# Performance work log

Measured on AMD Instinct MI355X. Metric: run time of the kernel, lower is better.

## Reference

```python
import jax, jax.numpy as jnp
import numpy as np

N_LAT, N_LON = 121, 240
N = N_LAT * N_LON          # 29040 nodes (fixed by module's reshape)
DEG = 16
E = N * DEG                # 464640 edges
H = 128                    # input_nf = output_nf = hidden_nf
LV = 11                    # pressure levels (coord_mlp outputs 11*2)
EDGE_IN = 2 * H + 34       # source + target + w_diff(33) + edge_attr(1)


def setup_inputs() -> dict:
    key = jax.random.key(0)
    ks = jax.random.split(key, 18)
    def w(k, shape, s=0.05):
        return jax.random.normal(k, shape, dtype=jnp.float32) * s
    return {
        'h': w(ks[0], (N, H), 1.0),
        'u': w(ks[1], (N, LV), 1.0),
        'v': w(ks[2], (N, LV), 1.0),
        'edge_attr': w(ks[3], (E, 1), 1.0),
        # edge MLP: Linear(EDGE_IN,H) ReLU Linear(H,H) ReLU
        'W_e1': w(ks[4], (EDGE_IN, H)), 'b_e1': jnp.zeros((H,), jnp.float32),
        'W_e2': w(ks[5], (H, H)),       'b_e2': jnp.zeros((H,), jnp.float32),
        # node MLP: Linear(2H+H,H) ReLU Linear(H,H)
        'W_n1': w(ks[6], (3 * H, H)),   'b_n1': jnp.zeros((H,), jnp.float32),
        'W_n2': w(ks[7], (H, H)),       'b_n2': jnp.zeros((H,), jnp.float32),
        # coord MLP: Linear(H,H) ReLU Linear(H,22,bias=False) with tiny xavier gain
        'W_c1': w(ks[8], (H, H)),       'b_c1': jnp.zeros((H,), jnp.float32),
        'W_cl': w(ks[9], (H, 2 * LV), 0.001),
        'edge_index': jax.random.randint(ks[10], (2, E), 0, N, dtype=jnp.int32),
    }


def reference(h, u, v, edge_attr,
              W_e1, b_e1, W_e2, b_e2,
              W_n1, b_n1, W_n2, b_n2,
              W_c1, b_c1, W_cl,
              edge_index):
    row, col = edge_index[0], edge_index[1]

    # ---- coord2radial ----
    uc, vc = u[col], v[col]          # [E, LV]
    ur, vr = u[row], v[row]
    col_speed = jnp.sqrt(uc * uc + vc * vc)
    row_speed = jnp.sqrt(ur * ur + vr * vr)
    rel_dirt = (uc * ur + vc * vr) / (col_speed * row_speed)
    w_diff = jnp.concatenate([rel_dirt, col_speed, row_speed], axis=1)  # [E, 33]

    # ---- edge model ----
    edge_in = jnp.concatenate([h[row], h[col], w_diff, edge_attr], axis=1)  # [E, EDGE_IN]
    edge_feat = jax.nn.relu(jax.nn.relu(edge_in @ W_e1 + b_e1) @ W_e2 + b_e2)  # [E, H]

    # ---- node model (scatter-sum + lat-band mean pooling) ----
    agg = jax.ops.segment_sum(edge_feat, row, num_segments=N)  # [N, H]
    lat = agg.reshape(N_LAT, N_LON, H).mean(axis=1, keepdims=True)  # [121,1,H]
    lat_agg = jnp.broadcast_to(lat, (N_LAT, N_LON, H)).reshape(N, H)
    node_in = jnp.concatenate([h, agg, lat_agg], axis=1)  # [N, 3H]
    h_out = jax.nn.relu(node_in @ W_n1 + b_n1) @ W_n2 + b_n2 + h  # residual

    # ---- coord model (scatter-mean with clamp) ----
    ef = (jax.nn.relu(edge_feat @ W_c1 + b_c1) @ W_cl).reshape(E, 2, LV)
    radial = jnp.stack([uc, vc], axis=1)                 # [E, 2, LV]
    rad2 = jnp.sqrt(jnp.sum(radial * radial, axis=-1))   # [E, 2] (per-component magnitude)
    wind = ef * rad2[:, :, None]                         # [E, 2, LV]
    cnt = jnp.maximum(
        jax.ops.segment_sum(jnp.ones((E,), jnp.float32), row, num_segments=N), 1.0)[:, None]
    agg_u = jnp.clip(jax.ops.segment_sum(wind[:, 0, :], row, num_segments=N) / cnt, -100.0, 100.0)
    agg_v = jnp.clip(jax.ops.segment_sum(wind[:, 1, :], row, num_segments=N) / cnt, -100.0, 100.0)

    return h_out, agg_u, agg_v
```

## Files before the change

### kernel.cpp

```cpp
#include <hip/hip_runtime.h>
#include <hip/hip_bf16.h>
#include <math.h>

#define NN   29040
#define NLAT 121
#define NLON 240
#define HD   128
#define LVN  11
#define EE   464640

typedef __attribute__((ext_vector_type(8))) short short8;
typedef __attribute__((ext_vector_type(16))) float f16v;

#define OFF_WE1 0
#define OFF_WE2 40960
#define OFF_WC1 57344
#define OFF_WCL 73728
#define OFF_WN1 77824
#define OFF_WN2 126976
#define WP_SHORTS 143360

__device__ inline short f2b(float x) {
    union { __hip_bfloat16 b; short s; } v;
    v.b = __float2bfloat16(x);
    return v.s;
}
__device__ inline float b2f(unsigned short b) {
    union { unsigned u; float f; } v; v.u = ((unsigned)b) << 16;
    return v.f;
}

#define SB_HIST  1815
#define SB_HCAST 1815
#define SB_UV    114
#define SB_WP    70

__global__ __launch_bounds__(256)
void setup_kernel(const int* __restrict__ eidx, int* __restrict__ cnt,
                  const float* __restrict__ h, short* __restrict__ hb,
                  const float* __restrict__ u, const float* __restrict__ v,
                  short* __restrict__ uvb,
                  const float* __restrict__ We1, const float* __restrict__ We2,
                  const float* __restrict__ Wc1, const float* __restrict__ Wcl,
                  const float* __restrict__ Wn1, const float* __restrict__ Wn2,
                  short* __restrict__ wp)
{
    const int b = blockIdx.x, tid = threadIdx.x;
    if (b < SB_HIST) {
        int e = b * 256 + tid;
        atomicAdd(&cnt[eidx[e]], 1);
        return;
    }
    if (b < SB_HIST + SB_HCAST) {
        int idx = (b - SB_HIST) * 256 + tid;
        const float4* hf = (const float4*)h;
        float4 a = hf[idx * 2], c = hf[idx * 2 + 1];
        short8 o;
        o[0] = f2b(a.x); o[1] = f2b(a.y); o[2] = f2b(a.z); o[3] = f2b(a.w);
        o[4] = f2b(c.x); o[5] = f2b(c.y); o[6] = f2b(c.z); o[7] = f2b(c.w);
        ((short8*)hb)[idx] = o;
        return;
    }
    if (b < SB_HIST + SB_HCAST + SB_UV) {
        int n = (b - SB_HIST - SB_HCAST) * 256 + tid;
        if (n >= NN) return;
        short* r = uvb + (size_t)n * 40;
        float un = 0.f, vn = 0.f;
#pragma unroll
        for (int l = 0; l < LVN; ++l) {
            float uu = u[n * LVN + l], vv = v[n * LVN + l];
            float s = sqrtf(uu * uu + vv * vv);
            r[l]      = f2b(uu / s);
            r[11 + l] = f2b(vv / s);
            r[22 + l] = f2b(s);
            un += uu * uu; vn += vv * vv;
        }
        r[33] = f2b(sqrtf(un));
        r[34] = f2b(sqrtf(vn));
        r[35] = 0; r[36] = 0; r[37] = 0; r[38] = 0; r[39] = 0;
        return;
    }
    {
        int fg = (b - SB_HIST - SB_HCAST - SB_UV) * 4 + (tid >> 6);
        const int l = tid & 63;
        int kind, f, base;
        if (fg < 80)       { kind = 0; f = fg;       base = OFF_WE1; }
        else if (fg < 112) { kind = 1; f = fg - 80;  base = OFF_WE2; }
        else if (fg < 144) { kind = 2; f = fg - 112; base = OFF_WC1; }
        else if (fg < 152) { kind = 3; f = fg - 144; base = OFF_WCL; }
        else if (fg < 248) { kind = 4; f = fg - 152; base = OFF_WN1; }
        else               { kind = 5; f = fg - 248; base = OFF_WN2; }
        const int nfw = (kind == 3) ? 1 : 4;
        const int kf = f / nfw, nf = f % nfw;
        short* dst = wp + base + (size_t)f * 512 + l * 8;
        for (int i = 0; i < 8; ++i) {
            int k = kf * 16 + ((l >> 5) << 3) + i;
            int n = nf * 32 + (l & 31);
            float val = 0.f;
            if (kind == 0) {
                int r = (k < 33) ? (256 + k) : (k == 33 ? 289 : (k < 64 ? -1 : k - 64));
                if (r >= 0) val = We1[r * HD + n];
            } else if (kind == 1) val = We2[k * HD + n];
            else if (kind == 2)  val = Wc1[k * HD + n];
            else if (kind == 3)  { if (n < 22) val = Wcl[k * 22 + n]; }
            else if (kind == 4)  val = Wn1[k * HD + n];
            else                 val = Wn2[k * HD + n];
            dst[i] = f2b(val);
        }
    }
}

__global__ __launch_bounds__(1024)
void scan_kernel(const int* __restrict__ cnt, int* __restrict__ off)
{
    __shared__ int part[1024];
    const int tid = threadIdx.x;
    const int CH = 29;
    int lo = tid * CH, hi = min(lo + CH, NN);
    int s = 0;
    for (int i = lo; i < hi; ++i) s += cnt[i];
    part[tid] = s;
    __syncthreads();
    for (int d = 1; d < 1024; d <<= 1) {
        int vv = (tid >= d) ? part[tid - d] : 0;
        __syncthreads();
        part[tid] += vv;
        __syncthreads();
    }
    int run = (tid == 0) ? 0 : part[tid - 1];
    for (int i = lo; i < hi; ++i) { off[i] = run; run += cnt[i]; }
    if (tid == 1023) off[NN] = run;
}

__global__ __launch_bounds__(256)
void scatter_kernel(const int* __restrict__ eidx, const float* __restrict__ ea,
                    const int* __restrict__ off, int* __restrict__ cur,
                    int* __restrict__ rows_r, int* __restrict__ cols_r,
                    float* __restrict__ ear)
{
    int e = blockIdx.x * 256 + threadIdx.x;
    if (e >= EE) return;
    int row = eidx[e];
    int col = eidx[EE + e];
    float a = ea[e];
    int p = atomicAdd(&cur[row], 1);
    int idx = off[row] + p;
    rows_r[idx] = row;
    cols_r[idx] = col;
    ear[idx] = a;
}

template<int KF, int NFL, int NJ>
__device__ inline void gemm32_lds(const short* At, const short* Wp, int nf0,
                                  const float* bias, f16v* acc,
                                  int mrow, int colbase, int r31, int kh, int lane)
{
    const char* arow = (const char*)At + mrow * 256;
    const int sw = (mrow & 7) << 4;
#pragma unroll
    for (int j = 0; j < NJ; ++j) {
        float bv = bias ? bias[colbase + j * 32 + r31] : 0.f;
#pragma unroll
        for (int q = 0; q < 16; ++q) acc[j][q] = bv;
    }
#pragma unroll
    for (int kf = 0; kf < KF; ++kf) {
        short8 a = *(const short8*)(arow + ((kf * 32 + 16 * kh) ^ sw));
#pragma unroll
        for (int j = 0; j < NJ; ++j) {
            short8 bfr = *(const short8*)(Wp + (size_t)(kf * NFL + nf0 + j) * 512 + lane * 8);
            acc[j] = __builtin_amdgcn_mfma_f32_32x32x16_bf16(a, bfr, acc[j], 0, 0, 0);
        }
    }
}

template<int NJ>
__device__ inline void store32(short* tile, const f16v* acc, int rg, int colbase,
                               int r31, int kh, bool relu)
{
#pragma unroll
    for (int j = 0; j < NJ; ++j)
#pragma unroll
        for (int reg = 0; reg < 16; ++reg) {
            int row = rg * 32 + (reg & 3) + 8 * (reg >> 2) + 4 * kh;
            int cb2 = (colbase + j * 32 + r31) * 2;
            float vv = acc[j][reg];
            if (relu) vv = fmaxf(vv, 0.f);
            *(short*)((char*)tile + row * 256 + (cb2 ^ ((row & 7) << 4))) = f2b(vv);
        }
}

__global__ __launch_bounds__(256, 4)
void edge_mfma(const short* __restrict__ hb, const short* __restrict__ uvb,
               const int* __restrict__ rows_r, const int* __restrict__ cols_r,
               const float* __restrict__ ear,
               const float* __restrict__ be1, const float* __restrict__ be2,
               const float* __restrict__ bc1,
               const short* __restrict__ wp,
               float* __restrict__ agg, float* __restrict__ aggu,
               float* __restrict__ aggv)
{
    __shared__ short Twd[64 * 64];
    __shared__ short T1[64 * 128];
    __shared__ int   rows_s[64];
    __shared__ float radu_s[64], radv_s[64];

    const int tid = threadIdx.x, lane = tid & 63, w = tid >> 6;
    const int rg = w >> 1, cg = w & 1;
    const int e0 = blockIdx.x * 64;
    const int r31 = lane & 31, kh = lane >> 5;
    const int mrow = rg * 32 + r31;
    const int sw = (mrow & 7) << 4;
    const int colbase = cg * 64;

    int rowm = rows_r[e0 + mrow], colm = cols_r[e0 + mrow];
    const short* hr = hb + (size_t)rowm * HD + 8 * kh;
    const short* hc = hb + (size_t)colm * HD + 8 * kh;

    {
        const int m2 = tid >> 2, q = tid & 3;
        const int sw2 = (m2 & 7) << 4;
        int row2 = rows_r[e0 + m2], col2 = cols_r[e0 + m2];
        const short* rc = uvb + (size_t)col2 * 40;
        const short* rr = uvb + (size_t)row2 * 40;
        char* arow = (char*)(Twd + m2 * 64);
        short8 z = {0, 0, 0, 0, 0, 0, 0, 0};
        *(short8*)(arow + q * 32) = z;
        *(short8*)(arow + q * 32 + 16) = z;
        for (int l = q; l < LVN; l += 4) {
            float rel = b2f((unsigned short)rc[l]) * b2f((unsigned short)rr[l])
                      + b2f((unsigned short)rc[11 + l]) * b2f((unsigned short)rr[11 + l]);
            *(short*)(arow + ((2 * l) ^ sw2))        = f2b(rel);
            *(short*)(arow + ((2 * (11 + l)) ^ sw2)) = rc[22 + l];
            *(short*)(arow + ((2 * (22 + l)) ^ sw2)) = rr[22 + l];
        }
        if (q == 0) {
            rows_s[m2] = row2;
            radu_s[m2] = b2f((unsigned short)rc[33]);
            radv_s[m2] = b2f((unsigned short)rc[34]);
        }
        if (q == 3) *(short*)(arow + ((2 * 33) ^ sw2)) = f2b(ear[e0 + m2]);
    }
    __syncthreads();

    f16v acc[2];
#pragma unroll
    for (int j = 0; j < 2; ++j) {
        float bv = be1[colbase + j * 32 + r31];
#pragma unroll
        for (int q = 0; q < 16; ++q) acc[j][q] = bv;
    }
    {
        const char* awd = (const char*)(Twd + mrow * 64);
#pragma unroll
        for (int kf = 0; kf < 4; ++kf) {
            short8 a = *(const short8*)(awd + ((kf * 32 + 16 * kh) ^ sw));
#pragma unroll
            for (int j = 0; j < 2; ++j) {
                short8 bfr = *(const short8*)(wp + OFF_WE1 + (size_t)(kf * 4 + cg * 2 + j) * 512 + lane * 8);
                acc[j] = __builtin_amdgcn_mfma_f32_32x32x16_bf16(a, bfr, acc[j], 0, 0, 0);
            }
        }
#pragma unroll
        for (int s = 0; s < 8; ++s) {
            short8 a = *(const short8*)(hr + s * 16);
#pragma unroll
            for (int j = 0; j < 2; ++j) {
                short8 bfr = *(const short8*)(wp + OFF_WE1 + (size_t)((s + 4) * 4 + cg * 2 + j) * 512 + lane * 8);
                acc[j] = __builtin_amdgcn_mfma_f32_32x32x16_bf16(a, bfr, acc[j], 0, 0, 0);
            }
        }
#pragma unroll
        for (int s = 0; s < 8; ++s) {
            short8 a = *(const short8*)(hc + s * 16);
#pragma unroll
            for (int j = 0; j < 2; ++j) {
                short8 bfr = *(const short8*)(wp + OFF_WE1 + (size_t)((s + 12) * 4 + cg * 2 + j) * 512 + lane * 8);
                acc[j] = __builtin_amdgcn_mfma_f32_32x32x16_bf16(a, bfr, acc[j], 0, 0, 0);
            }
        }
    }
    store32<2>(T1, acc, rg, colbase, r31, kh, true);
    __syncthreads();

    gemm32_lds<8, 4, 2>(T1, wp + OFF_WE2, cg * 2, be2, acc, mrow, colbase, r31, kh, lane);
    __syncthreads();
    store32<2>(T1, acc, rg, colbase, r31, kh, true);
    __syncthreads();

    gemm32_lds<8, 4, 2>(T1, wp + OFF_WC1, cg * 2, bc1, acc, mrow, colbase, r31, kh, lane);

    {
        const int col = colbase + lane;
        const int m0 = rg * 32;
        int curr = rows_s[m0];
        float s = 0.f;
        for (int m = m0; m < m0 + 32; ++m) {
            int r = rows_s[m];
            float vv = b2f(*(const unsigned short*)((const char*)T1 + m * 256 + (((col & 127) * 2) ^ ((m & 7) << 4))));
            if (r != curr) { atomicAdd(&agg[(size_t)curr * HD + (col & 127)], s); s = 0.f; curr = r; }
            s += vv;
        }
        atomicAdd(&agg[(size_t)curr * HD + (col & 127)], s);
    }
    __syncthreads();
    store32<2>(T1, acc, rg, colbase, r31, kh, true);
    __syncthreads();

    if (cg == 0) {
        gemm32_lds<8, 1, 1>(T1, wp + OFF_WCL, 0, (const float*)nullptr, acc, mrow, 0, r31, kh, lane);
        float* O22 = (float*)Twd;
#pragma unroll
        for (int reg = 0; reg < 16; ++reg) {
            int row = rg * 32 + (reg & 3) + 8 * (reg >> 2) + 4 * kh;
            O22[row * 32 + r31] = acc[0][reg];
        }
        const int c = r31;
        if (c < 22) {
            const bool isU = c < LVN;
            const int lvl = isU ? c : c - LVN;
            float* dst = isU ? aggu : aggv;
            const float* radp = isU ? radu_s : radv_s;
            const int m0 = rg * 32 + kh * 16;
            int curr = rows_s[m0]; float s = 0.f;
            for (int m = m0; m < m0 + 16; ++m) {
                int r = rows_s[m];
                float vv = O22[m * 32 + c] * radp[m];
                if (r != curr) { atomicAdd(&dst[(size_t)curr * LVN + lvl], s); s = 0.f; curr = r; }
                s += vv;
            }
            atomicAdd(&dst[(size_t)curr * LVN + lvl], s);
        }
    }
}

__global__ __launch_bounds__(256)
void post_kernel(const float* __restrict__ agg, short* __restrict__ latb)
{
    const int b = blockIdx.x, tid = threadIdx.x;
    __shared__ float part[256];
    const int j = tid & 127, half = tid >> 7;
    float s = 0.f;
    for (int lon = half * 120; lon < (half + 1) * 120; ++lon)
        s += agg[((size_t)b * NLON + lon) * HD + j];
    part[tid] = s;
    __syncthreads();
    if (tid < 128)
        latb[(size_t)b * HD + tid] = f2b((part[tid] + part[128 + tid]) * (1.0f / NLON));
}

__global__ __launch_bounds__(512, 4)
void node_mfma(const short* __restrict__ hb, const float* __restrict__ h,
               const short* __restrict__ latb,
               const float* __restrict__ bn1, const float* __restrict__ bn2,
               const short* __restrict__ wp, float* __restrict__ out,
               float* __restrict__ aggu, float* __restrict__ aggv,
               const int* __restrict__ off)
{
    __shared__ short T1[128 * 128];
    const int tid = threadIdx.x, lane = tid & 63, w = tid >> 6;
    const int rg = w >> 1, cg = w & 1;
    const int r31 = lane & 31, kh = lane >> 5;
    const int mrow = rg * 32 + r31;
    const int sw = (mrow & 7) << 4;
    const int colbase = cg * 64;
    const int n0 = blockIdx.x * 128;
    const int n = n0 + mrow;
    const int nc = (n < NN) ? n : (NN - 1);
    const short* hp = hb + (size_t)nc * HD + 8 * kh;
    const float* ap = out + (size_t)nc * HD + 8 * kh;
    const short* lp = latb + (size_t)(nc / NLON) * HD + 8 * kh;

    f16v acc[2];
#pragma unroll
    for (int j = 0; j < 2; ++j) {
        float bv = bn1[colbase + j * 32 + r31];
#pragma unroll
        for (int q = 0; q < 16; ++q) acc[j][q] = bv;
    }
#pragma unroll
    for (int s = 0; s < 8; ++s) {
        short8 a = *(const short8*)(hp + s * 16);
#pragma unroll
        for (int j = 0; j < 2; ++j) {
            short8 bfr = *(const short8*)(wp + OFF_WN1 + (size_t)(s * 4 + cg * 2 + j) * 512 + lane * 8);
            acc[j] = __builtin_amdgcn_mfma_f32_32x32x16_bf16(a, bfr, acc[j], 0, 0, 0);
        }
    }
#pragma unroll
    for (int s = 0; s < 8; ++s) {
        short8 a;
#pragma unroll
        for (int q = 0; q < 8; ++q) a[q] = f2b(ap[s * 16 + q]);
#pragma unroll
        for (int j = 0; j < 2; ++j) {
            short8 bfr = *(const short8*)(wp + OFF_WN1 + (size_t)((s + 8) * 4 + cg * 2 + j) * 512 + lane * 8);
            acc[j] = __builtin_amdgcn_mfma_f32_32x32x16_bf16(a, bfr, acc[j], 0, 0, 0);
        }
    }
#pragma unroll
    for (int s = 0; s < 8; ++s) {
        short8 a = *(const short8*)(lp + s * 16);
#pragma unroll
        for (int j = 0; j < 2; ++j) {
            short8 bfr = *(const short8*)(wp + OFF_WN1 + (size_t)((s + 16) * 4 + cg * 2 + j) * 512 + lane * 8);
            acc[j] = __builtin_amdgcn_mfma_f32_32x32x16_bf16(a, bfr, acc[j], 0, 0, 0);
        }
    }
    store32<2>(T1, acc, rg, colbase, r31, kh, true);
    __syncthreads();
    gemm32_lds<8, 4, 2>(T1, wp + OFF_WN2, cg * 2, bn2, acc, mrow, colbase, r31, kh, lane);

#pragma unroll
    for (int j = 0; j < 2; ++j)
#pragma unroll
        for (int reg = 0; reg < 16; ++reg) {
            int row = rg * 32 + (reg & 3) + 8 * (reg >> 2) + 4 * kh;
            int gn = n0 + row;
            if (gn < NN) {
                int col = colbase + j * 32 + r31;
                out[(size_t)gn * HD + col] = acc[j][reg] + h[(size_t)gn * HD + col];
            }
        }

    for (int tt = blockIdx.x * 512 + tid; tt < NN * LVN; tt += gridDim.x * 512) {
        int nn2 = tt / LVN;
        float c = fmaxf((float)(off[nn2 + 1] - off[nn2]), 1.f);
        float xu = aggu[tt] / c, xv = aggv[tt] / c;
        aggu[tt] = fminf(fmaxf(xu, -100.f), 100.f);
        aggv[tt] = fminf(fmaxf(xv, -100.f), 100.f);
    }
}

extern "C" void kernel_launch(void* const* d_in, const int* in_sizes, int n_in,
                              void* d_out, int out_size, void* d_ws, size_t ws_size,
                              hipStream_t stream)
{
    const float* h   = (const float*)d_in[0];
    const float* u   = (const float*)d_in[1];
    const float* v   = (const float*)d_in[2];
    const float* ea  = (const float*)d_in[3];
    const float* We1 = (const float*)d_in[4];
    const float* be1 = (const float*)d_in[5];
    const float* We2 = (const float*)d_in[6];
    const float* be2 = (const float*)d_in[7];
    const float* Wn1 = (const float*)d_in[8];
    const float* bn1 = (const float*)d_in[9];
    const float* Wn2 = (const float*)d_in[10];
    const float* bn2 = (const float*)d_in[11];
    const float* Wc1 = (const float*)d_in[12];
    const float* bc1 = (const float*)d_in[13];
    const float* Wcl = (const float*)d_in[14];
    const int*   eidx = (const int*)d_in[15];

    float* out  = (float*)d_out;
    float* agg  = out;
    float* aggu = out + (size_t)NN * HD;
    float* aggv = aggu + (size_t)NN * LVN;

    char* p = (char*)d_ws;
    short* wp  = (short*)p;                  p += (size_t)WP_SHORTS * 2;
    int*   off = (int*)p;                    p += (size_t)(NN + 1) * 4;
    p = (char*)(((size_t)p + 15) & ~(size_t)15);
    short* hb  = (short*)p;                  p += (size_t)NN * HD * 2;
    short* uvb = (short*)p;                  p += (size_t)NN * 40 * 2;
    short* latb = (short*)p;                 p += (size_t)NLAT * HD * 2;
    p = (char*)(((size_t)p + 15) & ~(size_t)15);
    int*   rows_r = (int*)p;                 p += (size_t)EE * 4;
    int*   cols_r = (int*)p;                 p += (size_t)EE * 4;
    float* ear    = (float*)p;               p += (size_t)EE * 4;
    p = (char*)(((size_t)p + 15) & ~(size_t)15);
    int*   cnt = (int*)p;                    p += (size_t)NN * 4;
    int*   cur = (int*)p;

    hipMemsetAsync(d_out, 0, (size_t)out_size * sizeof(float), stream);
    hipMemsetAsync(cnt, 0, (size_t)2 * NN * sizeof(int), stream);

    setup_kernel<<<SB_HIST + SB_HCAST + SB_UV + SB_WP, 256, 0, stream>>>(
        eidx, cnt, h, hb, u, v, uvb, We1, We2, Wc1, Wcl, Wn1, Wn2, wp);
    scan_kernel<<<1, 1024, 0, stream>>>(cnt, off);
    scatter_kernel<<<EE / 256, 256, 0, stream>>>(eidx, ea, off, cur,
                                                 rows_r, cols_r, ear);

    edge_mfma<<<EE / 64, 256, 0, stream>>>(hb, uvb, rows_r, cols_r, ear,
                                           be1, be2, bc1, wp, agg, aggu, aggv);

    post_kernel<<<NLAT, 256, 0, stream>>>(agg, latb);

    node_mfma<<<(NN + 127) / 128, 512, 0, stream>>>(hb, h, latb, bn1, bn2, wp,
                                                    agg, aggu, aggv, off);
}
```

Measured before the change: 287.1 us.

## Regroup setup work with scatter and remap edge blocks per XCD for L2 locality

The histogram now runs alone, and the bf16 casts of h, u/v and the weights move out of that launch and into a combined scatter+setup kernel that runs after the scan. Edge-kernel block indices are remapped so each of the 8 XCDs processes a contiguous range of sorted edges, which should improve L2 reuse of row-gathered node data. The node kernel now reads counts directly instead of differencing offsets. Costs are a changed launch composition and an XCD mapping that assumes round-robin dispatch across 8 XCDs.

After: 286.8 us. Within noise of the previous version (-0.1%).

```diff
diff --git a/kernel.cpp b/kernel.cpp
--- a/kernel.cpp
+++ b/kernel.cpp
@@ -30,29 +30,68 @@
     return v.f;
 }
 
-#define SB_HIST  1815
-#define SB_HCAST 1815
-#define SB_UV    114
-#define SB_WP    70
-
 __global__ __launch_bounds__(256)
-void setup_kernel(const int* __restrict__ eidx, int* __restrict__ cnt,
-                  const float* __restrict__ h, short* __restrict__ hb,
-                  const float* __restrict__ u, const float* __restrict__ v,
-                  short* __restrict__ uvb,
-                  const float* __restrict__ We1, const float* __restrict__ We2,
-                  const float* __restrict__ Wc1, const float* __restrict__ Wcl,
-                  const float* __restrict__ Wn1, const float* __restrict__ Wn2,
-                  short* __restrict__ wp)
+void hist_kernel(const int* __restrict__ eidx, int* __restrict__ cnt)
+{
+    int e = blockIdx.x * 256 + threadIdx.x;
+    atomicAdd(&cnt[eidx[e]], 1);
+}
+
+__global__ __launch_bounds__(1024)
+void scan_kernel(const int* __restrict__ cnt, int* __restrict__ off)
+{
+    __shared__ int part[1024];
+    const int tid = threadIdx.x;
+    const int CH = 29;
+    int lo = tid * CH, hi = min(lo + CH, NN);
+    int s = 0;
+    for (int i = lo; i < hi; ++i) s += cnt[i];
+    part[tid] = s;
+    __syncthreads();
+    for (int d = 1; d < 1024; d <<= 1) {
+        int vv = (tid >= d) ? part[tid - d] : 0;
+        __syncthreads();
+        part[tid] += vv;
+        __syncthreads();
+    }
+    int run = (tid == 0) ? 0 : part[tid - 1];
+    for (int i = lo; i < hi; ++i) { off[i] = run; run += cnt[i]; }
+    if (tid == 1023) off[NN] = run;
+}
+
+#define SS_SCAT  1815
+#define SS_HCAST 1815
+#define SS_UV    114
+#define SS_WP    70
+
+__global__ __launch_bounds__(256)
+void scatter_setup(const int* __restrict__ eidx, const float* __restrict__ ea,
+                   const int* __restrict__ off, int* __restrict__ cur,
+                   int* __restrict__ rows_r, int* __restrict__ cols_r,
+                   float* __restrict__ ear,
+                   const float* __restrict__ h, short* __restrict__ hb,
+                   const float* __restrict__ u, const float* __restrict__ v,
+                   short* __restrict__ uvb,
+                   const float* __restrict__ We1, const float* __restrict__ We2,
+                   const float* __restrict__ Wc1, const float* __restrict__ Wcl,
+                   const float* __restrict__ Wn1, const float* __restrict__ Wn2,
+                   short* __restrict__ wp)
 {
     const int b = blockIdx.x, tid = threadIdx.x;
-    if (b < SB_HIST) {
+    if (b < SS_SCAT) {
         int e = b * 256 + tid;
-        atomicAdd(&cnt[eidx[e]], 1);
+        int row = eidx[e];
+        int col = eidx[EE + e];
+        float a = ea[e];
+        int p = atomicAdd(&cur[row], 1);
+        int idx = off[row] + p;
+        rows_r[idx] = row;
+        cols_r[idx] = col;
+        ear[idx] = a;
         return;
     }
-    if (b < SB_HIST + SB_HCAST) {
-        int idx = (b - SB_HIST) * 256 + tid;
+    if (b < SS_SCAT + SS_HCAST) {
+        int idx = (b - SS_SCAT) * 256 + tid;
         const float4* hf = (const float4*)h;
         float4 a = hf[idx * 2], c = hf[idx * 2 + 1];
         short8 o;
@@ -61,8 +100,8 @@
         ((short8*)hb)[idx] = o;
         return;
     }
-    if (b < SB_HIST + SB_HCAST + SB_UV) {
-        int n = (b - SB_HIST - SB_HCAST) * 256 + tid;
+    if (b < SS_SCAT + SS_HCAST + SS_UV) {
+        int n = (b - SS_SCAT - SS_HCAST) * 256 + tid;
         if (n >= NN) return;
         short* r = uvb + (size_t)n * 40;
         float un = 0.f, vn = 0.f;
@@ -81,7 +120,7 @@
         return;
     }
     {
-        int fg = (b - SB_HIST - SB_HCAST - SB_UV) * 4 + (tid >> 6);
+        int fg = (b - SS_SCAT - SS_HCAST - SS_UV) * 4 + (tid >> 6);
         const int l = tid & 63;
         int kind, f, base;
         if (fg < 80)       { kind = 0; f = fg;       base = OFF_WE1; }
@@ -110,46 +149,6 @@
     }
 }
 
-__global__ __launch_bounds__(1024)
-void scan_kernel(const int* __restrict__ cnt, int* __restrict__ off)
-{
-    __shared__ int part[1024];
-    const int tid = threadIdx.x;
-    const int CH = 29;
-    int lo = tid * CH, hi = min(lo + CH, NN);
-    int s = 0;
-    for (int i = lo; i < hi; ++i) s += cnt[i];
-    part[tid] = s;
-    __syncthreads();
-    for (int d = 1; d < 1024; d <<= 1) {
-        int vv = (tid >= d) ? part[tid - d] : 0;
-        __syncthreads();
-        part[tid] += vv;
-        __syncthreads();
-    }
-    int run = (tid == 0) ? 0 : part[tid - 1];
-    for (int i = lo; i < hi; ++i) { off[i] = run; run += cnt[i]; }
-    if (tid == 1023) off[NN] = run;
-}
-
-__global__ __launch_bounds__(256)
-void scatter_kernel(const int* __restrict__ eidx, const float* __restrict__ ea,
-                    const int* __restrict__ off, int* __restrict__ cur,
-                    int* __restrict__ rows_r, int* __restrict__ cols_r,
-                    float* __restrict__ ear)
-{
-    int e = blockIdx.x * 256 + threadIdx.x;
-    if (e >= EE) return;
-    int row = eidx[e];
-    int col = eidx[EE + e];
-    float a = ea[e];
-    int p = atomicAdd(&cur[row], 1);
-    int idx = off[row] + p;
-    rows_r[idx] = row;
-    cols_r[idx] = col;
-    ear[idx] = a;
-}
-
 template<int KF, int NFL, int NJ>
 __device__ inline void gemm32_lds(const short* At, const short* Wp, int nf0,
                                   const float* bias, f16v* acc,
@@ -207,7 +206,10 @@
 
     const int tid = threadIdx.x, lane = tid & 63, w = tid >> 6;
     const int rg = w >> 1, cg = w & 1;
-    const int e0 = blockIdx.x * 64;
+    const int bid = blockIdx.x;
+    const int xcd = bid & 7, o = bid >> 3;
+    const int tbase = (xcd < 4) ? xcd * 908 : 4 * 908 + (xcd - 4) * 907;
+    const int e0 = (tbase + o) * 64;
     const int r31 = lane & 31, kh = lane >> 5;
     const int mrow = rg * 32 + r31;
     const int sw = (mrow & 7) << 4;
@@ -355,7 +357,7 @@
                const float* __restrict__ bn1, const float* __restrict__ bn2,
                const short* __restrict__ wp, float* __restrict__ out,
                float* __restrict__ aggu, float* __restrict__ aggv,
-               const int* __restrict__ off)
+               const int* __restrict__ cnt)
 {
     __shared__ short T1[128 * 128];
     const int tid = threadIdx.x, lane = tid & 63, w = tid >> 6;
@@ -425,7 +427,7 @@
 
     for (int tt = blockIdx.x * 512 + tid; tt < NN * LVN; tt += gridDim.x * 512) {
         int nn2 = tt / LVN;
-        float c = fmaxf((float)(off[nn2 + 1] - off[nn2]), 1.f);
+        float c = fmaxf((float)cnt[nn2], 1.f);
         float xu = aggu[tt] / c, xv = aggv[tt] / c;
         aggu[tt] = fminf(fmaxf(xu, -100.f), 100.f);
         aggv[tt] = fminf(fmaxf(xv, -100.f), 100.f);
@@ -476,11 +478,11 @@
     hipMemsetAsync(d_out, 0, (size_t)out_size * sizeof(float), stream);
     hipMemsetAsync(cnt, 0, (size_t)2 * NN * sizeof(int), stream);
 
-    setup_kernel<<<SB_HIST + SB_HCAST + SB_UV + SB_WP, 256, 0, stream>>>(
-        eidx, cnt, h, hb, u, v, uvb, We1, We2, Wc1, Wcl, Wn1, Wn2, wp);
+    hist_kernel<<<EE / 256, 256, 0, stream>>>(eidx, cnt);
     scan_kernel<<<1, 1024, 0, stream>>>(cnt, off);
-    scatter_kernel<<<EE / 256, 256, 0, stream>>>(eidx, ea, off, cur,
-                                                 rows_r, cols_r, ear);
+    scatter_setup<<<SS_SCAT + SS_HCAST + SS_UV + SS_WP, 256, 0, stream>>>(
+        eidx, ea, off, cur, rows_r, cols_r, ear,
+        h, hb, u, v, uvb, We1, We2, Wc1, Wcl, Wn1, Wn2, wp);
 
     edge_mfma<<<EE / 64, 256, 0, stream>>>(hb, uvb, rows_r, cols_r, ear,
                                            be1, be2, bc1, wp, agg, aggu, aggv);
@@ -488,5 +490,5 @@
     post_kernel<<<NLAT, 256, 0, stream>>>(agg, latb);
 
     node_mfma<<<(NN + 127) / 128, 512, 0, stream>>>(hb, h, latb, bn1, bn2, wp,
-                                                    agg, aggu, aggv, off);
-}
+                                                    agg, aggu, aggv, cnt);
+}
```
